# Kernel tuning notes

Hardware: AMD Instinct MI355X
Metric: run time of the kernel (lower is better)

## Reference

```python
import jax, jax.numpy as jnp
import numpy as np

IN_FEATURES_LS = (32, 64, 128, 256)
OUT_FEATURES = 1024
B, T = 16, 4096


def setup_inputs() -> dict:
    key = jax.random.key(0)
    k_x, k_idx, k_w, k_b = jax.random.split(key, 4)
    n = len(IN_FEATURES_LS)
    x = jax.random.normal(k_x, (B, T, OUT_FEATURES), dtype=jnp.float32)
    # per-row declared feature size, drawn from the configured list
    branch_idx = jax.random.randint(k_idx, (B, T), 0, n)
    in_feat_size = jnp.array(IN_FEATURES_LS, dtype=jnp.int32)[branch_idx]
    # kaiming_uniform_(a=sqrt(5)) on (n, out, out): fan_in = out, bound = 1/sqrt(fan_in)
    bound_w = 1.0 / np.sqrt(OUT_FEATURES)
    weight = jax.random.uniform(k_w, (n, OUT_FEATURES, OUT_FEATURES), dtype=jnp.float32,
                                minval=-bound_w, maxval=bound_w)
    bound_b = 1.0 / np.sqrt(OUT_FEATURES)
    bias = jax.random.uniform(k_b, (n, OUT_FEATURES), dtype=jnp.float32,
                              minval=-bound_b, maxval=bound_b)
    return {"x": x, "in_feat_size": in_feat_size, "weight": weight, "bias": bias}


def reference(x, in_feat_size, weight, bias):
    # Loop over the small fixed set of feature-size branches (matches original).
    out = jnp.zeros(x.shape[:-1] + (OUT_FEATURES,), dtype=x.dtype)
    for idx, feat_size in enumerate(IN_FEATURES_LS):
        mask = (in_feat_size == feat_size)[..., None].astype(x.dtype)  # [B,T,1]
        y = jnp.einsum('oi,bti->bto', weight[idx], x) + bias[idx]
        out = out + mask * y
    return out
```

## Files before the change

### kernel.cpp

```cpp
#include <hip/hip_runtime.h>
#include <hip/hip_bf16.h>

#define OUTF 1024
#define NROWS 65536
#define NBR 4
#define XBROWS 66560
#define NWG 4160

typedef __attribute__((ext_vector_type(8))) short short8;
typedef __attribute__((ext_vector_type(4))) float f32x4;

__device__ inline unsigned short f2bf(float f) {
    return __builtin_bit_cast(unsigned short, (__bf16)f);
}
__device__ inline void gload_lds16(const void* g, void* l) {
    __builtin_amdgcn_global_load_lds(
        (const __attribute__((address_space(1))) void*)g,
        (__attribute__((address_space(3))) void*)l, 16, 0, 0);
}
__device__ inline short8 pack8(float4 a, float4 b) {
    short8 o;
    o[0] = (short)f2bf(a.x); o[1] = (short)f2bf(a.y);
    o[2] = (short)f2bf(a.z); o[3] = (short)f2bf(a.w);
    o[4] = (short)f2bf(b.x); o[5] = (short)f2bf(b.y);
    o[6] = (short)f2bf(b.z); o[7] = (short)f2bf(b.w);
    return o;
}
__device__ inline short8 pack8v(f32x4 a, f32x4 b) {
    short8 o;
    o[0] = (short)f2bf(a[0]); o[1] = (short)f2bf(a[1]);
    o[2] = (short)f2bf(a[2]); o[3] = (short)f2bf(a[3]);
    o[4] = (short)f2bf(b[0]); o[5] = (short)f2bf(b[1]);
    o[6] = (short)f2bf(b[2]); o[7] = (short)f2bf(b[3]);
    return o;
}

__global__ void k_count(const int* __restrict__ feat, int* __restrict__ cnt) {
    __shared__ int lc[NBR];
    int tid = threadIdx.x;
    if (tid < NBR) lc[tid] = 0;
    __syncthreads();
    int r = blockIdx.x * 256 + tid;
    int b = 26 - __clz(feat[r]);
    atomicAdd(&lc[b], 1);
    __syncthreads();
    if (tid < NBR && lc[tid]) atomicAdd(&cnt[tid], lc[tid]);
}

__global__ void k_prefix(int* __restrict__ ws) {
    if (threadIdx.x == 0) {
        int s = 0;
        for (int b = 0; b < NBR; b++) {
            ws[4 + b] = s;
            s = (s + ws[b] + 255) & ~255;
            ws[8 + b] = 0;
        }
    }
}

__global__ void k_fill(const int* __restrict__ feat, int* __restrict__ ws,
                       int* __restrict__ rowlist) {
    int tid = threadIdx.x;
    int lane = tid & 63;
    int r = blockIdx.x * 256 + tid;
    int b = 26 - __clz(feat[r]);
    #pragma unroll
    for (int bb = 0; bb < NBR; bb++) {
        unsigned long long mask = __ballot(b == bb);
        int leader = __ffsll((long long)mask) - 1;
        int cntw = __popcll(mask);
        int basepos = 0;
        if (lane == leader) basepos = atomicAdd(&ws[8 + bb], cntw);
        basepos = __shfl(basepos, leader < 0 ? 0 : leader);
        if (b == bb) {
            int prefix = __popcll(mask & ((1ull << lane) - 1ull));
            rowlist[ws[4 + bb] + basepos + prefix] = r;
        }
    }
}

__global__ void k_convw(const float* __restrict__ w, unsigned short* __restrict__ wsw) {
    int idx = (int)blockIdx.x * 256 + (int)threadIdx.x;
    int branch = idx >> 17;
    int rem = idx & 131071;
    int n = rem >> 7;
    int cb = (rem & 127) << 4;
    int kw = cb >> 7;
    int wb_ = cb & 127;
    int src = kw * 64 + ((wb_ ^ ((n & 7) << 4)) >> 1);
    const float4* s = reinterpret_cast<const float4*>(
        w + ((size_t)branch << 20) + (size_t)n * OUTF + src);
    char* dst = reinterpret_cast<char*>(wsw) + ((size_t)branch << 21) + (size_t)n * 2048 + cb;
    *reinterpret_cast<short8*>(dst) = pack8(s[0], s[1]);
}

__global__ __launch_bounds__(256, 3)
void k_gemm7(const float* __restrict__ x,
             const unsigned short* __restrict__ wsw,
             const float* __restrict__ bias,
             const int* __restrict__ ws_i,
             const int* __restrict__ rowlist,
             float* __restrict__ out) {
    __shared__ char Alds[32768];
    __shared__ char Blds[16384];

    const int d = (int)blockIdx.x;
    const int work = (d & 7) * (NWG >> 3) + (d >> 3);
    const int mtile = work >> 3;
    const int ntile = work & 7;

    int branch = -1, lt = 0, cnt = 0, rbase = 0;
    int t_ = mtile;
    #pragma unroll
    for (int b = 0; b < NBR; b++) {
        if (branch < 0) {
            int c = ws_i[b];
            int nt = (c + 127) >> 7;
            if (t_ < nt) { branch = b; lt = t_; cnt = c; rbase = ws_i[4 + b]; }
            else t_ -= nt;
        }
    }
    if (branch < 0) return;

    const int tid = (int)threadIdx.x;
    const int lane = tid & 63;
    const int wid = tid >> 6;
    const int wm = (wid & 1) << 6;
    const int wn = (wid >> 1) << 6;
    const int n0 = ntile << 7;
    const int row0 = rbase + (lt << 7);

    const char* aP[8];
    {
        const int rsub = tid >> 4;
        const int sc = ((tid & 15) << 4) ^ ((rsub & 7) << 4);
        #pragma unroll
        for (int i = 0; i < 8; i++) {
            int rl = rowlist[row0 + i * 16 + rsub];
            if ((unsigned)rl >= NROWS) rl = 0;
            aP[i] = reinterpret_cast<const char*>(x + (size_t)rl * OUTF) + sc;
        }
    }
    const char* bP[4];
    #pragma unroll
    for (int i = 0; i < 4; i++) {
        int rn = i * 32 + (tid >> 3);
        bP[i] = reinterpret_cast<const char*>(wsw) + ((size_t)branch << 21)
                + (size_t)(n0 + rn) * 2048 + ((tid & 7) << 4);
    }
    const int dst16 = tid << 4;

    f32x4 acc[4][4];
    #pragma unroll
    for (int i = 0; i < 4; i++)
        #pragma unroll
        for (int j = 0; j < 4; j++) acc[i][j] = (f32x4){0.f, 0.f, 0.f, 0.f};

    const int q = lane >> 4;
    const int lr = lane & 15;

    for (int kt = 0; kt < 16; ++kt) {
        #pragma unroll
        for (int i = 0; i < 8; i++)
            gload_lds16(aP[i] + kt * 256, Alds + i * 4096 + dst16);
        #pragma unroll
        for (int i = 0; i < 4; i++)
            gload_lds16(bP[i] + kt * 128, Blds + i * 4096 + dst16);
        __syncthreads();

        #pragma unroll
        for (int ks = 0; ks < 2; ks++) {
            short8 af[4], bfr[4];
            #pragma unroll
            for (int i = 0; i < 4; i++) {
                const int r = wm + i * 16 + lr;
                const int off = ((ks << 7) + (q << 5)) ^ ((r & 7) << 4);
                const f32x4 v0 = *reinterpret_cast<const f32x4*>(Alds + r * 256 + off);
                const f32x4 v1 = *reinterpret_cast<const f32x4*>(Alds + r * 256 + (off ^ 16));
                af[i] = pack8v(v0, v1);
            }
            #pragma unroll
            for (int j = 0; j < 4; j++) {
                const int r = wn + j * 16 + lr;
                const int off = ((ks << 6) + (q << 4)) ^ ((r & 7) << 4);
                bfr[j] = *reinterpret_cast<const short8*>(Blds + r * 128 + off);
            }
            __builtin_amdgcn_s_setprio(1);
            #pragma unroll
            for (int i = 0; i < 4; i++)
                #pragma unroll
                for (int j = 0; j < 4; j++)
                    acc[i][j] = __builtin_amdgcn_mfma_f32_16x16x32_bf16(af[i], bfr[j], acc[i][j], 0, 0, 0);
            __builtin_amdgcn_s_setprio(0);
        }
        __syncthreads();
    }

    const int ccol = lane & 15;
    const int crow = (lane >> 4) << 2;
    float bv[4];
    const float* bp = bias + branch * OUTF + n0 + wn;
    #pragma unroll
    for (int fn = 0; fn < 4; fn++) bv[fn] = bp[fn * 16 + ccol];
    #pragma unroll
    for (int fm = 0; fm < 4; fm++) {
        #pragma unroll
        for (int j = 0; j < 4; j++) {
            int gm = (lt << 7) + wm + fm * 16 + crow + j;
            if (gm < cnt) {
                int orow = rowlist[rbase + gm];
                float* orp = out + (size_t)orow * OUTF + n0 + wn;
                #pragma unroll
                for (int fn = 0; fn < 4; fn++)
                    orp[fn * 16 + ccol] = acc[fm][fn][j] + bv[fn];
            }
        }
    }
}

__global__ __launch_bounds__(256, 3)
void k_gemm_fb(const float* __restrict__ x,
               const float* __restrict__ wf,
               const float* __restrict__ bias,
               const int* __restrict__ ws_i,
               const int* __restrict__ rowlist,
               float* __restrict__ out) {
    __shared__ unsigned short As[128][72];
    __shared__ unsigned short Bs[128][72];

    int t = (int)blockIdx.x;
    int branch = -1, ltile = 0, cnt = 0, rbase = 0;
    #pragma unroll
    for (int b = 0; b < NBR; b++) {
        if (branch < 0) {
            int c = ws_i[b];
            int nt = (c + 127) >> 7;
            if (t < nt) { branch = b; ltile = t; cnt = c; rbase = ws_i[4 + b]; }
            else t -= nt;
        }
    }
    if (branch < 0) return;

    const int tid = threadIdx.x;
    const int lane = tid & 63;
    const int wid = tid >> 6;
    const int wm = (wid & 1) << 6;
    const int wn = (wid >> 1) << 6;
    const int n0 = (int)blockIdx.y * 128;

    const int srow = tid >> 1;
    const int scol = (tid & 1) << 5;

    const int gmrow = ltile * 128 + srow;
    const int grow = (gmrow < cnt) ? rowlist[rbase + gmrow] : -1;
    const float* xsrc = x + (size_t)(grow < 0 ? 0 : grow) * OUTF + scol;
    const float* wfsrc = wf + ((size_t)branch << 20) + (size_t)(n0 + srow) * OUTF + scol;

    f32x4 acc[4][4];
    #pragma unroll
    for (int i = 0; i < 4; i++)
        #pragma unroll
        for (int j = 0; j < 4; j++)
            acc[i][j] = (f32x4){0.f, 0.f, 0.f, 0.f};

    for (int k0 = 0; k0 < OUTF; k0 += 64) {
        {
            unsigned short* dst = &As[srow][scol];
            if (grow >= 0) {
                const float4* s4 = reinterpret_cast<const float4*>(xsrc + k0);
                #pragma unroll
                for (int i = 0; i < 8; i += 2)
                    *reinterpret_cast<short8*>(dst + i * 4) = pack8(s4[i], s4[i + 1]);
            } else {
                short8 z = (short8){0, 0, 0, 0, 0, 0, 0, 0};
                #pragma unroll
                for (int i = 0; i < 8; i += 2) *reinterpret_cast<short8*>(dst + i * 4) = z;
            }
        }
        {
            unsigned short* dst = &Bs[srow][scol];
            const float4* s4 = reinterpret_cast<const float4*>(wfsrc + k0);
            #pragma unroll
            for (int i = 0; i < 8; i += 2)
                *reinterpret_cast<short8*>(dst + i * 4) = pack8(s4[i], s4[i + 1]);
        }
        __syncthreads();
        #pragma unroll
        for (int kk = 0; kk < 64; kk += 32) {
            const int krd = kk + (lane >> 4) * 8;
            short8 af[4], bf_[4];
            #pragma unroll
            for (int i = 0; i < 4; i++)
                af[i] = *reinterpret_cast<const short8*>(&As[wm + i * 16 + (lane & 15)][krd]);
            #pragma unroll
            for (int i = 0; i < 4; i++)
                bf_[i] = *reinterpret_cast<const short8*>(&Bs[wn + i * 16 + (lane & 15)][krd]);
            #pragma unroll
            for (int i = 0; i < 4; i++)
                #pragma unroll
                for (int j = 0; j < 4; j++)
                    acc[i][j] = __builtin_amdgcn_mfma_f32_16x16x32_bf16(af[i], bf_[j], acc[i][j], 0, 0, 0);
        }
        __syncthreads();
    }

    const int ccol = lane & 15;
    const int crow = (lane >> 4) << 2;
    float bv[4];
    const float* bp = bias + branch * OUTF + n0 + wn;
    #pragma unroll
    for (int fn = 0; fn < 4; fn++) bv[fn] = bp[fn * 16 + ccol];
    #pragma unroll
    for (int fm = 0; fm < 4; fm++) {
        #pragma unroll
        for (int j = 0; j < 4; j++) {
            int gm = ltile * 128 + wm + fm * 16 + crow + j;
            if (gm < cnt) {
                int orow = rowlist[rbase + gm];
                float* orp = out + (size_t)orow * OUTF + n0 + wn;
                #pragma unroll
                for (int fn = 0; fn < 4; fn++)
                    orp[fn * 16 + ccol] = acc[fm][fn][j] + bv[fn];
            }
        }
    }
}

extern "C" void kernel_launch(void* const* d_in, const int* in_sizes, int n_in,
                              void* d_out, int out_size, void* d_ws, size_t ws_size,
                              hipStream_t stream) {
    const float* x = (const float*)d_in[0];
    const int* feat = (const int*)d_in[1];
    const float* w = (const float*)d_in[2];
    const float* bias = (const float*)d_in[3];
    float* out = (float*)d_out;

    char* ws = (char*)d_ws;
    int* ws_i = (int*)ws;
    int* rowlist = (int*)(ws + 256);
    const size_t WSW_OFF = (size_t)512 << 10;
    unsigned short* wsw = (unsigned short*)(ws + WSW_OFF);
    const size_t need = WSW_OFF + (size_t)NBR * OUTF * OUTF * 2;

    (void)hipMemsetAsync(ws_i, 0, 64, stream);
    k_count<<<NROWS / 256, 256, 0, stream>>>(feat, ws_i);
    k_prefix<<<1, 64, 0, stream>>>(ws_i);
    k_fill<<<NROWS / 256, 256, 0, stream>>>(feat, ws_i, rowlist);

    if (ws_size >= need) {
        k_convw<<<2048, 256, 0, stream>>>(w, wsw);
        k_gemm7<<<NWG, 256, 0, stream>>>(x, wsw, bias, ws_i, rowlist, out);
    } else {
        dim3 grid(NROWS / 128 + NBR, OUTF / 128);
        k_gemm_fb<<<grid, 256, 0, stream>>>(x, w, bias, ws_i, rowlist, out);
    }
}
```

Before: 338.7 us.

## Pre-convert gathered x rows to swizzled bf16 before GEMM

Adds a k_convx pass that gathers x rows in branch-sorted order, converts them to bf16 and writes them in the same XOR-swizzled layout as the weights. The GEMM then streams contiguous bf16 tiles for A as well as B. This halves the LDS footprint for A and removes the per-fragment fp32-to-bf16 packing from the MFMA loop. It also folds k_prefix into on-the-fly segment base computation, and moves the weight conversion earlier. The cost is an extra full read of x plus a bf16 write and a read-back, which adds global memory traffic.

```diff
diff --git a/kernel.cpp b/kernel.cpp
--- a/kernel.cpp
+++ b/kernel.cpp
@@ -5,7 +5,7 @@
 #define NROWS 65536
 #define NBR 4
 #define XBROWS 66560
-#define NWG 4160
+#define NWG 4128
 
 typedef __attribute__((ext_vector_type(8))) short short8;
 typedef __attribute__((ext_vector_type(4))) float f32x4;
@@ -26,13 +26,10 @@
     o[6] = (short)f2bf(b.z); o[7] = (short)f2bf(b.w);
     return o;
 }
-__device__ inline short8 pack8v(f32x4 a, f32x4 b) {
-    short8 o;
-    o[0] = (short)f2bf(a[0]); o[1] = (short)f2bf(a[1]);
-    o[2] = (short)f2bf(a[2]); o[3] = (short)f2bf(a[3]);
-    o[4] = (short)f2bf(b[0]); o[5] = (short)f2bf(b[1]);
-    o[6] = (short)f2bf(b[2]); o[7] = (short)f2bf(b[3]);
-    return o;
+__device__ inline void seg_bases(const int* __restrict__ ws_i, int* base) {
+    int s = 0;
+    #pragma unroll
+    for (int b = 0; b < NBR; b++) { base[b] = s; s = (s + ws_i[b] + 255) & ~255; }
 }
 
 __global__ void k_count(const int* __restrict__ feat, int* __restrict__ cnt) {
@@ -47,19 +44,10 @@
     if (tid < NBR && lc[tid]) atomicAdd(&cnt[tid], lc[tid]);
 }
 
-__global__ void k_prefix(int* __restrict__ ws) {
-    if (threadIdx.x == 0) {
-        int s = 0;
-        for (int b = 0; b < NBR; b++) {
-            ws[4 + b] = s;
-            s = (s + ws[b] + 255) & ~255;
-            ws[8 + b] = 0;
-        }
-    }
-}
-
 __global__ void k_fill(const int* __restrict__ feat, int* __restrict__ ws,
                        int* __restrict__ rowlist) {
+    int base[NBR];
+    seg_bases(ws, base);
     int tid = threadIdx.x;
     int lane = tid & 63;
     int r = blockIdx.x * 256 + tid;
@@ -74,7 +62,7 @@
         basepos = __shfl(basepos, leader < 0 ? 0 : leader);
         if (b == bb) {
             int prefix = __popcll(mask & ((1ull << lane) - 1ull));
-            rowlist[ws[4 + bb] + basepos + prefix] = r;
+            rowlist[base[bb] + basepos + prefix] = r;
         }
     }
 }
@@ -94,21 +82,38 @@
     *reinterpret_cast<short8*>(dst) = pack8(s[0], s[1]);
 }
 
+__global__ void k_convx(const float* __restrict__ x, const int* __restrict__ rowlist,
+                        unsigned short* __restrict__ xb) {
+    int g = (int)blockIdx.x * 512 + (int)threadIdx.x;
+    int orow = g >> 7;
+    int cb = (g & 127) << 4;
+    int rl = rowlist[orow];
+    if ((unsigned)rl >= NROWS) rl = 0;
+    int kw = cb >> 7;
+    int wb_ = cb & 127;
+    int src = kw * 64 + ((wb_ ^ ((orow & 7) << 4)) >> 1);
+    const float4* s = reinterpret_cast<const float4*>(x + (size_t)rl * OUTF + src);
+    *reinterpret_cast<short8*>(reinterpret_cast<char*>(xb) + (size_t)orow * 2048 + cb) =
+        pack8(s[0], s[1]);
+}
+
 __global__ __launch_bounds__(256, 3)
-void k_gemm7(const float* __restrict__ x,
-             const unsigned short* __restrict__ wsw,
-             const float* __restrict__ bias,
-             const int* __restrict__ ws_i,
-             const int* __restrict__ rowlist,
-             float* __restrict__ out) {
-    __shared__ char Alds[32768];
-    __shared__ char Blds[16384];
+void k_gemm11(const unsigned short* __restrict__ xb,
+              const unsigned short* __restrict__ wsw,
+              const float* __restrict__ bias,
+              const int* __restrict__ ws_i,
+              const int* __restrict__ rowlist,
+              float* __restrict__ out) {
+    __shared__ char As[16384];
+    __shared__ char Bs[16384];
 
     const int d = (int)blockIdx.x;
     const int work = (d & 7) * (NWG >> 3) + (d >> 3);
     const int mtile = work >> 3;
     const int ntile = work & 7;
 
+    int bases[NBR];
+    seg_bases(ws_i, bases);
     int branch = -1, lt = 0, cnt = 0, rbase = 0;
     int t_ = mtile;
     #pragma unroll
@@ -116,7 +121,7 @@
         if (branch < 0) {
             int c = ws_i[b];
             int nt = (c + 127) >> 7;
-            if (t_ < nt) { branch = b; lt = t_; cnt = c; rbase = ws_i[4 + b]; }
+            if (t_ < nt) { branch = b; lt = t_; cnt = c; rbase = bases[b]; }
             else t_ -= nt;
         }
     }
@@ -130,24 +135,10 @@
     const int n0 = ntile << 7;
     const int row0 = rbase + (lt << 7);
 
-    const char* aP[8];
-    {
-        const int rsub = tid >> 4;
-        const int sc = ((tid & 15) << 4) ^ ((rsub & 7) << 4);
-        #pragma unroll
-        for (int i = 0; i < 8; i++) {
-            int rl = rowlist[row0 + i * 16 + rsub];
-            if ((unsigned)rl >= NROWS) rl = 0;
-            aP[i] = reinterpret_cast<const char*>(x + (size_t)rl * OUTF) + sc;
-        }
-    }
-    const char* bP[4];
-    #pragma unroll
-    for (int i = 0; i < 4; i++) {
-        int rn = i * 32 + (tid >> 3);
-        bP[i] = reinterpret_cast<const char*>(wsw) + ((size_t)branch << 21)
-                + (size_t)(n0 + rn) * 2048 + ((tid & 7) << 4);
-    }
+    const char* aS = reinterpret_cast<const char*>(xb)
+                     + (size_t)(row0 + (tid >> 3)) * 2048 + ((tid & 7) << 4);
+    const char* bS = reinterpret_cast<const char*>(wsw) + ((size_t)branch << 21)
+                     + (size_t)(n0 + (tid >> 3)) * 2048 + ((tid & 7) << 4);
     const int dst16 = tid << 4;
 
     f32x4 acc[4][4];
@@ -156,41 +147,37 @@
         #pragma unroll
         for (int j = 0; j < 4; j++) acc[i][j] = (f32x4){0.f, 0.f, 0.f, 0.f};
 
+    const int lr = lane & 15;
     const int q = lane >> 4;
-    const int lr = lane & 15;
+    const int swz = (lane & 7) << 4;
+    const int arowb = (wm + lr) << 7;
+    const int browb = (wn + lr) << 7;
 
     for (int kt = 0; kt < 16; ++kt) {
         #pragma unroll
-        for (int i = 0; i < 8; i++)
-            gload_lds16(aP[i] + kt * 256, Alds + i * 4096 + dst16);
-        #pragma unroll
         for (int i = 0; i < 4; i++)
-            gload_lds16(bP[i] + kt * 128, Blds + i * 4096 + dst16);
+            gload_lds16(aS + (size_t)i * 65536 + kt * 128, As + i * 4096 + dst16);
+        #pragma unroll
+        for (int i = 0; i < 4; i++)
+            gload_lds16(bS + (size_t)i * 65536 + kt * 128, Bs + i * 4096 + dst16);
         __syncthreads();
 
         #pragma unroll
         for (int ks = 0; ks < 2; ks++) {
-            short8 af[4], bfr[4];
-            #pragma unroll
-            for (int i = 0; i < 4; i++) {
-                const int r = wm + i * 16 + lr;
-                const int off = ((ks << 7) + (q << 5)) ^ ((r & 7) << 4);
-                const f32x4 v0 = *reinterpret_cast<const f32x4*>(Alds + r * 256 + off);
-                const f32x4 v1 = *reinterpret_cast<const f32x4*>(Alds + r * 256 + (off ^ 16));
-                af[i] = pack8v(v0, v1);
-            }
-            #pragma unroll
-            for (int j = 0; j < 4; j++) {
-                const int r = wn + j * 16 + lr;
-                const int off = ((ks << 6) + (q << 4)) ^ ((r & 7) << 4);
-                bfr[j] = *reinterpret_cast<const short8*>(Blds + r * 128 + off);
-            }
+            const int kb = (ks << 6) + (q << 4);
+            short8 af[4], bf_[4];
+            #pragma unroll
+            for (int i = 0; i < 4; i++)
+                af[i] = *reinterpret_cast<const short8*>(As + arowb + (i << 11) + (kb ^ swz));
+            #pragma unroll
+            for (int j = 0; j < 4; j++)
+                bf_[j] = *reinterpret_cast<const short8*>(Bs + browb + (j << 11) + (kb ^ swz));
             __builtin_amdgcn_s_setprio(1);
             #pragma unroll
             for (int i = 0; i < 4; i++)
                 #pragma unroll
                 for (int j = 0; j < 4; j++)
-                    acc[i][j] = __builtin_amdgcn_mfma_f32_16x16x32_bf16(af[i], bfr[j], acc[i][j], 0, 0, 0);
+                    acc[i][j] = __builtin_amdgcn_mfma_f32_16x16x32_bf16(af[i], bf_[j], acc[i][j], 0, 0, 0);
             __builtin_amdgcn_s_setprio(0);
         }
         __syncthreads();
@@ -228,6 +215,8 @@
     __shared__ unsigned short As[128][72];
     __shared__ unsigned short Bs[128][72];
 
+    int bases[NBR];
+    seg_bases(ws_i, bases);
     int t = (int)blockIdx.x;
     int branch = -1, ltile = 0, cnt = 0, rbase = 0;
     #pragma unroll
@@ -235,7 +224,7 @@
         if (branch < 0) {
             int c = ws_i[b];
             int nt = (c + 127) >> 7;
-            if (t < nt) { branch = b; ltile = t; cnt = c; rbase = ws_i[4 + b]; }
+            if (t < nt) { branch = b; ltile = t; cnt = c; rbase = bases[b]; }
             else t -= nt;
         }
     }
@@ -252,8 +241,9 @@
     const int scol = (tid & 1) << 5;
 
     const int gmrow = ltile * 128 + srow;
-    const int grow = (gmrow < cnt) ? rowlist[rbase + gmrow] : -1;
-    const float* xsrc = x + (size_t)(grow < 0 ? 0 : grow) * OUTF + scol;
+    int grl = (gmrow < cnt) ? rowlist[rbase + gmrow] : -1;
+    if (grl >= NROWS) grl = -1;
+    const float* xsrc = x + (size_t)(grl < 0 ? 0 : grl) * OUTF + scol;
     const float* wfsrc = wf + ((size_t)branch << 20) + (size_t)(n0 + srow) * OUTF + scol;
 
     f32x4 acc[4][4];
@@ -266,7 +256,7 @@
     for (int k0 = 0; k0 < OUTF; k0 += 64) {
         {
             unsigned short* dst = &As[srow][scol];
-            if (grow >= 0) {
+            if (grl >= 0) {
                 const float4* s4 = reinterpret_cast<const float4*>(xsrc + k0);
                 #pragma unroll
                 for (int i = 0; i < 8; i += 2)
@@ -339,17 +329,20 @@
     int* ws_i = (int*)ws;
     int* rowlist = (int*)(ws + 256);
     const size_t WSW_OFF = (size_t)512 << 10;
+    const size_t XB_OFF = (size_t)9 << 20;
     unsigned short* wsw = (unsigned short*)(ws + WSW_OFF);
-    const size_t need = WSW_OFF + (size_t)NBR * OUTF * OUTF * 2;
+    unsigned short* xb = (unsigned short*)(ws + XB_OFF);
+    const size_t need_full = XB_OFF + (size_t)XBROWS * 2048;
 
     (void)hipMemsetAsync(ws_i, 0, 64, stream);
+    if (ws_size >= need_full)
+        k_convw<<<2048, 256, 0, stream>>>(w, wsw);
     k_count<<<NROWS / 256, 256, 0, stream>>>(feat, ws_i);
-    k_prefix<<<1, 64, 0, stream>>>(ws_i);
     k_fill<<<NROWS / 256, 256, 0, stream>>>(feat, ws_i, rowlist);
 
-    if (ws_size >= need) {
-        k_convw<<<2048, 256, 0, stream>>>(w, wsw);
-        k_gemm7<<<NWG, 256, 0, stream>>>(x, wsw, bias, ws_i, rowlist, out);
+    if (ws_size >= need_full) {
+        k_convx<<<(XBROWS * 128) / 512, 512, 0, stream>>>(x, rowlist, xb);
+        k_gemm11<<<NWG, 256, 0, stream>>>(xb, wsw, bias, ws_i, rowlist, out);
     } else {
         dim3 grid(NROWS / 128 + NBR, OUTF / 128);
         k_gemm_fb<<<grid, 256, 0, stream>>>(x, w, bias, ws_i, rowlist, out);
```

New measurement: 337.2 us. No clear change (-0.5%).
